# Optimization experiments

Measured on AMD Instinct MI355X. Metric: run time of the kernel, lower is better.

Reference implementation:

```python
import jax, jax.numpy as jnp
import numpy as np

B, S, H = 2, 2048, 2048
NH, KVH, HD = 32, 8, 64
G = NH // KVH
BASE = 10000.0
SCALE = 1.0 / np.sqrt(HD).astype(np.float32)


def _rope_cache(seq_len, dim, base):
    inv_freq = 1.0 / (base ** (jnp.arange(0, dim, 2, dtype=jnp.float32) / dim))
    t = jnp.arange(seq_len, dtype=jnp.float32)
    freqs = jnp.outer(t, inv_freq)            # [S, HD/2]
    emb = jnp.concatenate([freqs, freqs], -1)  # [S, HD]
    return jnp.cos(emb), jnp.sin(emb)


def _rotate_half(x):
    x1, x2 = jnp.split(x, 2, axis=-1)
    return jnp.concatenate([-x2, x1], axis=-1)


def setup_inputs() -> dict:
    key = jax.random.key(0)
    ks = jax.random.split(key, 5)
    hidden_states = jax.random.normal(ks[0], (B, S, H), jnp.float32)
    # additive causal mask, broadcast over heads
    causal = jnp.tril(jnp.ones((S, S), dtype=bool))
    attention_mask = jnp.where(causal, 0.0, -1e9).astype(jnp.float32)[None, None]
    attention_mask = jnp.broadcast_to(attention_mask, (B, 1, S, S))
    position_ids = jnp.broadcast_to(jnp.arange(S, dtype=jnp.int32), (B, S))
    w = 0.02
    Wq = jax.random.normal(ks[1], (H, NH * HD), jnp.float32) * w
    Wk = jax.random.normal(ks[2], (H, KVH * HD), jnp.float32) * w
    Wv = jax.random.normal(ks[3], (H, KVH * HD), jnp.float32) * w
    Wo = jax.random.normal(ks[4], (NH * HD, H), jnp.float32) * w
    return {"hidden_states": hidden_states, "attention_mask": attention_mask,
            "position_ids": position_ids, "Wq": Wq, "Wk": Wk, "Wv": Wv, "Wo": Wo}


def reference(hidden_states, attention_mask, position_ids, Wq, Wk, Wv, Wo):
    b, s, _ = hidden_states.shape
    q = (hidden_states @ Wq).reshape(b, s, NH, HD).transpose(0, 2, 1, 3)   # [B,NH,S,HD]
    k = (hidden_states @ Wk).reshape(b, s, KVH, HD).transpose(0, 2, 1, 3)  # [B,KVH,S,HD]
    v = (hidden_states @ Wv).reshape(b, s, KVH, HD).transpose(0, 2, 1, 3)
    cos_c, sin_c = _rope_cache(s, HD, BASE)
    cos = cos_c[position_ids][:, None]  # [B,1,S,HD]
    sin = sin_c[position_ids][:, None]
    q = q * cos + _rotate_half(q) * sin
    k = k * cos + _rotate_half(k) * sin
    # GQA: grouped einsum == repeat_kv + matmul (same math, no KV duplication)
    qg = q.reshape(b, KVH, G, s, HD)
    scores = jnp.einsum('bkgsd,bktd->bkgst', qg, k) * SCALE  # [B,KVH,G,S,S]
    scores = scores + attention_mask[:, :, None]             # mask [B,1,1,S,S]
    probs = jax.nn.softmax(scores.astype(jnp.float32), axis=-1).astype(q.dtype)
    ctx = jnp.einsum('bkgst,bktd->bkgsd', probs, v)
    ctx = ctx.reshape(b, NH, s, HD).transpose(0, 2, 1, 3).reshape(b, s, NH * HD)
    return ctx @ Wo
```

## Files before the change

kernel.cpp:

```cpp
#include <hip/hip_runtime.h>
#include <hip/hip_bf16.h>

#define DB   2
#define DS   2048
#define DH   2048
#define DNH  32
#define DKVH 8
#define DHD  64
#define DM   4096
#define DNQKV 3072

typedef __attribute__((ext_vector_type(8))) short bf16x8;
typedef __attribute__((ext_vector_type(4))) float f32x4;
typedef __attribute__((ext_vector_type(8))) unsigned short us8;
typedef __attribute__((ext_vector_type(4))) unsigned short us4;

__device__ __forceinline__ float b2f(unsigned short u) {
  unsigned int x = ((unsigned int)u) << 16;
  return __builtin_bit_cast(float, x);
}
__device__ __forceinline__ unsigned short f2b(float f) {
  unsigned int u = __builtin_bit_cast(unsigned int, f);
  return (unsigned short)((u + 0x8000u) >> 16);
}
__device__ __forceinline__ void async_copy16(void* lds, const void* g) {
  __builtin_amdgcn_global_load_lds((const __attribute__((address_space(1))) void*)g,
                                   (__attribute__((address_space(3))) void*)lds,
                                   16, 0, 0);
}

__global__ void detect_mode(const unsigned short* __restrict__ w, int* __restrict__ flags) {
  int t = threadIdx.x;
  int trips = 0;
  for (int i = 0; i < 4; i++) {
    unsigned short u = w[t * 4 + i];
    int e = (u >> 7) & 0xFF;
    if (e >= 161 || (e <= 93 && e != 0)) trips++;
  }
  for (int off = 32; off > 0; off >>= 1) trips += __shfl_down(trips, off);
  if (t == 0) flags[0] = (trips >= 8) ? 1 : 0;
}

__global__ __launch_bounds__(256) void convert_x(const void* __restrict__ xin,
                                                 unsigned short* __restrict__ xb,
                                                 const int* __restrict__ flags, int n) {
  int mode = flags[0];
  int i = (blockIdx.x * 256 + threadIdx.x) * 8;
  if (i >= n) return;
  if (mode) {
    const float* f = (const float*)xin;
    us8 o;
#pragma unroll
    for (int j = 0; j < 8; j++) o[j] = f2b(f[i + j]);
    *(us8*)&xb[i] = o;
  } else {
    *(us8*)&xb[i] = *(const us8*)((const unsigned short*)xin + i);
  }
}

__global__ __launch_bounds__(256) void transpose_w(const void* __restrict__ win,
                                                   unsigned short* __restrict__ out,
                                                   const int* __restrict__ flags,
                                                   int R, int C) {
  __shared__ float tile[32][33];
  int mode = flags[0];
  int c0 = blockIdx.x * 32, r0 = blockIdx.y * 32;
  int tx = threadIdx.x & 31, ty = threadIdx.x >> 5;
  if (mode) {
    const float* f = (const float*)win;
    for (int i = ty; i < 32; i += 8) tile[i][tx] = f[(size_t)(r0 + i) * C + c0 + tx];
  } else {
    const unsigned short* bsrc = (const unsigned short*)win;
    for (int i = ty; i < 32; i += 8) tile[i][tx] = b2f(bsrc[(size_t)(r0 + i) * C + c0 + tx]);
  }
  __syncthreads();
  for (int i = ty; i < 32; i += 8) out[(size_t)(c0 + i) * R + r0 + tx] = f2b(tile[tx][i]);
}

#define QSC 0.18033688011112042f

__global__ __launch_bounds__(256)
void gemm_qkv(const unsigned short* __restrict__ A, const unsigned short* __restrict__ Bt,
              const int* __restrict__ pos_ids,
              unsigned short* __restrict__ qws, unsigned short* __restrict__ kws,
              unsigned short* __restrict__ vt) {
  __shared__ __align__(16) unsigned short lA[2 * 128 * 32];
  __shared__ __align__(16) unsigned short lB[2 * 128 * 32];
  int tid = threadIdx.x, lane = tid & 63, wave = tid >> 6;
  int wm = wave >> 1, wn = wave & 1;
  int quad = lane >> 4, l15 = lane & 15;
  size_t tm0 = (size_t)blockIdx.y * 128, tn0 = (size_t)blockIdx.x * 128;

  f32x4 zero4 = {0.f, 0.f, 0.f, 0.f};
  f32x4 acc[4][4];
#pragma unroll
  for (int mi = 0; mi < 4; mi++)
#pragma unroll
    for (int ni = 0; ni < 4; ni++) acc[mi][ni] = zero4;

  for (int kt = 0; kt < 32; kt++) {
    __syncthreads();
#pragma unroll
    for (int i = 0; i < 4; i++) {
      int c = tid + 256 * i;
      int col = (c & 3) * 8;
      int r = (c >> 2) & 127;
      int half = c >> 9;
      async_copy16(&lA[c * 8], A + (tm0 + r) * DH + kt * 64 + half * 32 + col);
      async_copy16(&lB[c * 8], Bt + (tn0 + r) * DH + kt * 64 + half * 32 + col);
    }
    __syncthreads();
#pragma unroll
    for (int ks = 0; ks < 2; ks++) {
      bf16x8 af[4], bfr[4];
#pragma unroll
      for (int mi = 0; mi < 4; mi++)
        af[mi] = *(const bf16x8*)&lA[ks * 4096 + (wm * 64 + mi * 16 + l15) * 32 + quad * 8];
#pragma unroll
      for (int ni = 0; ni < 4; ni++)
        bfr[ni] = *(const bf16x8*)&lB[ks * 4096 + (wn * 64 + ni * 16 + l15) * 32 + quad * 8];
#pragma unroll
      for (int mi = 0; mi < 4; mi++)
#pragma unroll
        for (int ni = 0; ni < 4; ni++)
          acc[mi][ni] = __builtin_amdgcn_mfma_f32_16x16x32_bf16(af[mi], bfr[ni], acc[mi][ni], 0, 0, 0);
    }
  }

  int hs = (int)(tn0 >> 6) + wn;
  if (hs < 40) {
    float sc = (hs < 32) ? QSC : 1.0f;
    unsigned short* dst0 = (hs < 32) ? qws : kws;
    int hh = (hs < 32) ? hs : (hs - 32);
    float invf0 = __expf(-(float)l15 * (9.210340371976184f / 32.0f));
    float invf1 = invf0 * 0.01f;
#pragma unroll
    for (int mi = 0; mi < 4; mi++)
#pragma unroll
      for (int r = 0; r < 4; r++) {
        size_t gr = tm0 + wm * 64 + mi * 16 + quad * 4 + r;
        int b = (int)(gr >> 11), s = (int)(gr & 2047);
        float t = (float)pos_ids[gr];
        unsigned short* row = dst0 + ((size_t)(b * ((hs < 32) ? DNH : DKVH) + hh) * DS + s) * DHD;
#pragma unroll
        for (int ni = 0; ni < 2; ni++) {
          float x1 = acc[mi][ni][r], x2 = acc[mi][ni + 2][r];
          float ang = t * (ni ? invf1 : invf0);
          float sn, cs;
          __sincosf(ang, &sn, &cs);
          int d = ni * 16 + l15;
          row[d]      = f2b((x1 * cs - x2 * sn) * sc);
          row[d + 32] = f2b((x2 * cs + x1 * sn) * sc);
        }
      }
  } else {
    int vh = hs - 40;
    int b = (int)(tm0 >> 11);
    int s0 = (int)(tm0 & 2047) + wm * 64 + quad * 4;
#pragma unroll
    for (int mi = 0; mi < 4; mi++)
#pragma unroll
      for (int ni = 0; ni < 4; ni++) {
        int d = ni * 16 + l15;
        us4 o4;
#pragma unroll
        for (int r = 0; r < 4; r++) o4[r] = f2b(acc[mi][ni][r]);
        *(us4*)&vt[((size_t)(b * DKVH + vh) * DHD + d) * DS + s0 + mi * 16] = o4;
      }
  }
}

__global__ __launch_bounds__(256)
void gemm_out(const unsigned short* __restrict__ A, const unsigned short* __restrict__ Bt,
              unsigned short* __restrict__ Cb, float* __restrict__ Cf,
              const int* __restrict__ outmode) {
  __shared__ __align__(16) unsigned short lA[2 * 128 * 32];
  __shared__ __align__(16) unsigned short lB[2 * 128 * 32];
  int tid = threadIdx.x, lane = tid & 63, wave = tid >> 6;
  int wm = wave >> 1, wn = wave & 1;
  int quad = lane >> 4, l15 = lane & 15;
  size_t tm0 = (size_t)blockIdx.y * 128, tn0 = (size_t)blockIdx.x * 128;

  f32x4 zero4 = {0.f, 0.f, 0.f, 0.f};
  f32x4 acc[4][4];
#pragma unroll
  for (int mi = 0; mi < 4; mi++)
#pragma unroll
    for (int ni = 0; ni < 4; ni++) acc[mi][ni] = zero4;

  for (int kt = 0; kt < 32; kt++) {
    __syncthreads();
#pragma unroll
    for (int i = 0; i < 4; i++) {
      int c = tid + 256 * i;
      int col = (c & 3) * 8;
      int r = (c >> 2) & 127;
      int half = c >> 9;
      async_copy16(&lA[c * 8], A + (tm0 + r) * DH + kt * 64 + half * 32 + col);
      async_copy16(&lB[c * 8], Bt + (tn0 + r) * DH + kt * 64 + half * 32 + col);
    }
    __syncthreads();
#pragma unroll
    for (int ks = 0; ks < 2; ks++) {
      bf16x8 af[4], bfr[4];
#pragma unroll
      for (int mi = 0; mi < 4; mi++)
        af[mi] = *(const bf16x8*)&lA[ks * 4096 + (wm * 64 + mi * 16 + l15) * 32 + quad * 8];
#pragma unroll
      for (int ni = 0; ni < 4; ni++)
        bfr[ni] = *(const bf16x8*)&lB[ks * 4096 + (wn * 64 + ni * 16 + l15) * 32 + quad * 8];
#pragma unroll
      for (int mi = 0; mi < 4; mi++)
#pragma unroll
        for (int ni = 0; ni < 4; ni++)
          acc[mi][ni] = __builtin_amdgcn_mfma_f32_16x16x32_bf16(af[mi], bfr[ni], acc[mi][ni], 0, 0, 0);
    }
  }
  int mode = *outmode;
#pragma unroll
  for (int mi = 0; mi < 4; mi++)
#pragma unroll
    for (int ni = 0; ni < 4; ni++)
#pragma unroll
      for (int r = 0; r < 4; r++) {
        size_t gr = tm0 + wm * 64 + mi * 16 + quad * 4 + r;
        size_t gc = tn0 + wn * 64 + ni * 16 + l15;
        float v = acc[mi][ni][r];
        if (mode) Cf[gr * DH + gc] = v;
        else      Cb[gr * DH + gc] = f2b(v);
      }
}

__global__ __launch_bounds__(256, 4)
void flash_attn(const unsigned short* __restrict__ q, const unsigned short* __restrict__ k,
                const unsigned short* __restrict__ vt, unsigned short* __restrict__ ctx) {
  __shared__ __align__(16) unsigned short lK0[64 * 32];
  __shared__ __align__(16) unsigned short lK1[64 * 32];
  __shared__ __align__(16) unsigned short lV0[64 * 32];
  __shared__ __align__(16) unsigned short lV1[64 * 32];
  __shared__ __align__(16) unsigned short lP[4 * 16 * 72];
  int tid = threadIdx.x, lane = tid & 63, wave = tid >> 6;
  int quad = lane >> 4, l15 = lane & 15;
  int bh = blockIdx.y, b = bh >> 5, h = bh & 31, kvh = h >> 2;
  const unsigned short* qb = q + (size_t)(b * DNH + h) * DS * DHD;
  const unsigned short* kb = k + (size_t)(b * DKVH + kvh) * DS * DHD;
  const unsigned short* vb = vt + (size_t)(b * DKVH + kvh) * DHD * DS;
  unsigned short* lPw = lP + wave * 16 * 72;
  int r4 = tid >> 2, c8 = (tid & 3) * 8;

  f32x4 zero4 = {0.f, 0.f, 0.f, 0.f};
  for (int ph = 0; ph < 2; ph++) {
    int qt = ph ? (31 - blockIdx.x) : blockIdx.x;
    int q0 = qt * 64;
    const unsigned short* qp = qb + (size_t)(q0 + wave * 16 + l15) * DHD + quad * 8;
    bf16x8 qf0 = *(const bf16x8*)qp;
    bf16x8 qf1 = *(const bf16x8*)(qp + 32);
    f32x4 oacc[4];
#pragma unroll
    for (int dj = 0; dj < 4; dj++) oacc[dj] = zero4;
    float mrow = -1e30f, lrow = 0.f;

    int nt = qt + 1;
    for (int t = 0; t < nt; t++) {
      int kv0 = t * 64;
      __syncthreads();
      async_copy16(&lK0[tid * 8], kb + (size_t)(kv0 + r4) * DHD + c8);
      async_copy16(&lK1[tid * 8], kb + (size_t)(kv0 + r4) * DHD + 32 + c8);
      async_copy16(&lV0[tid * 8], vb + (size_t)r4 * DS + kv0 + c8);
      async_copy16(&lV1[tid * 8], vb + (size_t)r4 * DS + kv0 + 32 + c8);
      __syncthreads();

      f32x4 sacc[4];
#pragma unroll
      for (int nj = 0; nj < 4; nj++) {
        sacc[nj] = zero4;
        bf16x8 kf0 = *(const bf16x8*)&lK0[(nj * 16 + l15) * 32 + quad * 8];
        bf16x8 kf1 = *(const bf16x8*)&lK1[(nj * 16 + l15) * 32 + quad * 8];
        sacc[nj] = __builtin_amdgcn_mfma_f32_16x16x32_bf16(kf0, qf0, sacc[nj], 0, 0, 0);
        sacc[nj] = __builtin_amdgcn_mfma_f32_16x16x32_bf16(kf1, qf1, sacc[nj], 0, 0, 0);
      }
      if (t == nt - 1) {
        int ql = wave * 16 + l15;
#pragma unroll
        for (int nj = 0; nj < 4; nj++)
#pragma unroll
          for (int r = 0; r < 4; r++)
            if (nj * 16 + quad * 4 + r > ql) sacc[nj][r] = -1e30f;
      }
      float tm = -1e30f;
#pragma unroll
      for (int nj = 0; nj < 4; nj++)
#pragma unroll
        for (int r = 0; r < 4; r++) tm = fmaxf(tm, sacc[nj][r]);
      tm = fmaxf(tm, __shfl_xor(tm, 16));
      tm = fmaxf(tm, __shfl_xor(tm, 32));
      float mn = fmaxf(mrow, tm);
      float alpha = __builtin_amdgcn_exp2f(mrow - mn);
      mrow = mn;
      float rs = 0.f;
      float p[4][4];
#pragma unroll
      for (int nj = 0; nj < 4; nj++)
#pragma unroll
        for (int r = 0; r < 4; r++) {
          float e = __builtin_amdgcn_exp2f(sacc[nj][r] - mn);
          p[nj][r] = e;
          rs += e;
        }
      rs += __shfl_xor(rs, 16);
      rs += __shfl_xor(rs, 32);
      lrow = lrow * alpha + rs;
#pragma unroll
      for (int nj = 0; nj < 4; nj++) {
        us4 w4;
#pragma unroll
        for (int r = 0; r < 4; r++) w4[r] = f2b(p[nj][r]);
        *(us4*)&lPw[l15 * 72 + nj * 16 + quad * 4] = w4;
      }
      bf16x8 pf0 = *(const bf16x8*)&lPw[l15 * 72 + quad * 8];
      bf16x8 pf1 = *(const bf16x8*)&lPw[l15 * 72 + 32 + quad * 8];
#pragma unroll
      for (int dj = 0; dj < 4; dj++) {
#pragma unroll
        for (int r = 0; r < 4; r++) oacc[dj][r] *= alpha;
        bf16x8 vf0 = *(const bf16x8*)&lV0[(dj * 16 + l15) * 32 + quad * 8];
        bf16x8 vf1 = *(const bf16x8*)&lV1[(dj * 16 + l15) * 32 + quad * 8];
        oacc[dj] = __builtin_amdgcn_mfma_f32_16x16x32_bf16(vf0, pf0, oacc[dj], 0, 0, 0);
        oacc[dj] = __builtin_amdgcn_mfma_f32_16x16x32_bf16(vf1, pf1, oacc[dj], 0, 0, 0);
      }
    }
    float inv = __builtin_amdgcn_rcpf(lrow);
    size_t orow = ((size_t)b * DS + q0 + wave * 16 + l15) * (DNH * DHD) + (size_t)h * DHD;
#pragma unroll
    for (int dj = 0; dj < 4; dj++) {
      us4 o4;
#pragma unroll
      for (int r = 0; r < 4; r++) o4[r] = f2b(oacc[dj][r] * inv);
      *(us4*)&ctx[orow + dj * 16 + quad * 4] = o4;
    }
  }
}

extern "C" void kernel_launch(void* const* d_in, const int* in_sizes, int n_in,
                              void* d_out, int out_size, void* d_ws, size_t ws_size,
                              hipStream_t stream) {
  (void)in_sizes; (void)n_in; (void)out_size; (void)ws_size;
  const void* hs = d_in[0];
  const int* pos = (const int*)d_in[2];
  const void* wq = d_in[3];
  const void* wk = d_in[4];
  const void* wv = d_in[5];
  const void* wo = d_in[6];

  char* ws = (char*)d_ws;
  size_t off = 0;
  auto take = [&](size_t bytes) -> char* {
    char* p = ws + off;
    off += (bytes + 255) & ~(size_t)255;
    return p;
  };
  int* flags            = (int*)take(256);
  unsigned short* xb    = (unsigned short*)take((size_t)DM * DH * 2);
  unsigned short* wtqkv = (unsigned short*)take((size_t)DNQKV * DH * 2);
  unsigned short* wto   = (unsigned short*)take((size_t)DH * DH * 2);
  unsigned short* qws   = (unsigned short*)take((size_t)DB * DNH * DS * DHD * 2);
  unsigned short* kws   = (unsigned short*)take((size_t)DB * DKVH * DS * DHD * 2);
  unsigned short* vtws  = (unsigned short*)take((size_t)DB * DKVH * DS * DHD * 2);
  unsigned short* ctx   = (unsigned short*)take((size_t)DM * DNH * DHD * 2);

  detect_mode<<<1, 64, 0, stream>>>((const unsigned short*)wq, flags);
  convert_x<<<DM * DH / 8 / 256, 256, 0, stream>>>(hs, xb, flags, DM * DH);
  transpose_w<<<dim3(64, 64), 256, 0, stream>>>(wq, wtqkv, flags, 2048, 2048);
  transpose_w<<<dim3(16, 64), 256, 0, stream>>>(wk, wtqkv + (size_t)2048 * 2048, flags, 2048, 512);
  transpose_w<<<dim3(16, 64), 256, 0, stream>>>(wv, wtqkv + (size_t)2560 * 2048, flags, 2048, 512);
  transpose_w<<<dim3(64, 64), 256, 0, stream>>>(wo, wto, flags, 2048, 2048);

  gemm_qkv<<<dim3(24, 32), 256, 0, stream>>>(xb, wtqkv, pos, qws, kws, vtws);

  flash_attn<<<dim3(16, DB * DNH), 256, 0, stream>>>(qws, kws, vtws, ctx);

  gemm_out<<<dim3(16, 32), 256, 0, stream>>>(ctx, wto, (unsigned short*)d_out, (float*)d_out, flags);
}
```

Measured before the change: 357.1 us.

## Rewrite QKV and output GEMMs with larger tiles and pipelined double-buffered LDS

Both projection GEMMs move to 512-thread blocks with larger tiles (256x256 for QKV, 128x256 for output). Global-to-LDS loads are double-buffered across K-steps and split into half-tiles interleaved with MFMA phases, using explicit vmcnt waits and s_setprio. The change also adds an XOR swizzle on LDS to avoid bank conflicts and remaps block IDs for L2 locality. It aims to hide memory latency and raise MFMA utilization. The cost is many barriers, heavy register pressure (acc[8][4] in QKV) and fewer blocks (192 and 256), which may leave CUs idle.

```diff
diff --git a/kernel.cpp b/kernel.cpp
--- a/kernel.cpp
+++ b/kernel.cpp
@@ -28,6 +28,11 @@
                                    (__attribute__((address_space(3))) void*)lds,
                                    16, 0, 0);
 }
+
+#define BARRIER() do { asm volatile("" ::: "memory"); __builtin_amdgcn_s_barrier(); asm volatile("" ::: "memory"); } while (0)
+#define LGKM0()   asm volatile("s_waitcnt lgkmcnt(0)" ::: "memory")
+#define WAITVM(n) asm volatile("s_waitcnt vmcnt(" #n ")" ::: "memory")
+#define MFMA16(d, a, bb) (d) = __builtin_amdgcn_mfma_f32_16x16x32_bf16((a), (bb), (d), 0, 0, 0)
 
 __global__ void detect_mode(const unsigned short* __restrict__ w, int* __restrict__ flags) {
   int t = threadIdx.x;
@@ -79,53 +84,115 @@
 
 #define QSC 0.18033688011112042f
 
-__global__ __launch_bounds__(256)
+__global__ __launch_bounds__(512, 2)
 void gemm_qkv(const unsigned short* __restrict__ A, const unsigned short* __restrict__ Bt,
               const int* __restrict__ pos_ids,
               unsigned short* __restrict__ qws, unsigned short* __restrict__ kws,
               unsigned short* __restrict__ vt) {
-  __shared__ __align__(16) unsigned short lA[2 * 128 * 32];
-  __shared__ __align__(16) unsigned short lB[2 * 128 * 32];
+  __shared__ __align__(16) unsigned short sm[65536];
   int tid = threadIdx.x, lane = tid & 63, wave = tid >> 6;
-  int wm = wave >> 1, wn = wave & 1;
+  int wm = wave >> 2, wn = wave & 3;
   int quad = lane >> 4, l15 = lane & 15;
-  size_t tm0 = (size_t)blockIdx.y * 128, tn0 = (size_t)blockIdx.x * 128;
+
+  int bid = blockIdx.x;
+  int wg = (bid & 7) * 24 + (bid >> 3);
+  int ty = wg / 12, tx = wg - ty * 12;
+  size_t tm0 = (size_t)ty * 256, tn0 = (size_t)tx * 256;
+
+  const unsigned short* Ab = A + tm0 * 2048;
+  const unsigned short* Bb = Bt + tn0 * 2048;
+
+  auto UA = [&](int bu, int kh) { return sm + (bu * 2 + kh) * 8192; };
+  auto UB = [&](int bu, int kh) { return sm + 32768 + (bu * 2 + kh) * 8192; };
+
+  int c0 = tid, c1 = tid + 512;
+  int r0s = c0 >> 2, r1s = c1 >> 2;
+  int cc0 = (c0 & 3) ^ ((r0s >> 1) & 3);
+  int cc1 = (c1 & 3) ^ ((r1s >> 1) & 3);
+  size_t ga0 = (size_t)r0s * 2048 + cc0 * 8;
+  size_t ga1 = (size_t)r1s * 2048 + cc1 * 8;
+
+  auto stA = [&](int t, int kh, int bu) {
+    const unsigned short* s = Ab + (size_t)t * 64 + kh * 32;
+    async_copy16(UA(bu, kh) + c0 * 8, s + ga0);
+    async_copy16(UA(bu, kh) + c1 * 8, s + ga1);
+  };
+  auto stB = [&](int t, int kh, int bu) {
+    const unsigned short* s = Bb + (size_t)t * 64 + kh * 32;
+    async_copy16(UB(bu, kh) + c0 * 8, s + ga0);
+    async_copy16(UB(bu, kh) + c1 * 8, s + ga1);
+  };
+
+  int rdoff = l15 * 32 + ((quad << 3) ^ (((l15 >> 1) & 3) << 3));
 
   f32x4 zero4 = {0.f, 0.f, 0.f, 0.f};
-  f32x4 acc[4][4];
-#pragma unroll
-  for (int mi = 0; mi < 4; mi++)
+  f32x4 acc[8][4];
+#pragma unroll
+  for (int mi = 0; mi < 8; mi++)
 #pragma unroll
     for (int ni = 0; ni < 4; ni++) acc[mi][ni] = zero4;
 
-  for (int kt = 0; kt < 32; kt++) {
-    __syncthreads();
-#pragma unroll
-    for (int i = 0; i < 4; i++) {
-      int c = tid + 256 * i;
-      int col = (c & 3) * 8;
-      int r = (c >> 2) & 127;
-      int half = c >> 9;
-      async_copy16(&lA[c * 8], A + (tm0 + r) * DH + kt * 64 + half * 32 + col);
-      async_copy16(&lB[c * 8], Bt + (tn0 + r) * DH + kt * 64 + half * 32 + col);
-    }
-    __syncthreads();
-#pragma unroll
-    for (int ks = 0; ks < 2; ks++) {
-      bf16x8 af[4], bfr[4];
-#pragma unroll
-      for (int mi = 0; mi < 4; mi++)
-        af[mi] = *(const bf16x8*)&lA[ks * 4096 + (wm * 64 + mi * 16 + l15) * 32 + quad * 8];
-#pragma unroll
-      for (int ni = 0; ni < 4; ni++)
-        bfr[ni] = *(const bf16x8*)&lB[ks * 4096 + (wn * 64 + ni * 16 + l15) * 32 + quad * 8];
-#pragma unroll
-      for (int mi = 0; mi < 4; mi++)
-#pragma unroll
-        for (int ni = 0; ni < 4; ni++)
-          acc[mi][ni] = __builtin_amdgcn_mfma_f32_16x16x32_bf16(af[mi], bfr[ni], acc[mi][ni], 0, 0, 0);
-    }
-  }
+  stA(0, 0, 0); stB(0, 0, 0); stA(0, 1, 0); stB(0, 1, 0); stA(1, 0, 1); stB(1, 0, 1);
+  WAITVM(8); BARRIER();
+
+#pragma unroll 2
+  for (int t = 0; t < 32; ++t) {
+    int bu = t & 1, bn = bu ^ 1;
+    int t1 = (t + 1 < 32) ? t + 1 : 31;
+    int t2 = (t + 2 < 32) ? t + 2 : 31;
+    bf16x8 af[8];
+    const unsigned short* pA0 = UA(bu, 0) + wm * 4096 + rdoff;
+    const unsigned short* pB0 = UB(bu, 0) + wn * 2048 + rdoff;
+    const unsigned short* pA1 = UA(bu, 1) + wm * 4096 + rdoff;
+    const unsigned short* pB1 = UB(bu, 1) + wn * 2048 + rdoff;
+
+#pragma unroll
+    for (int mi = 0; mi < 8; mi++) af[mi] = *(const bf16x8*)(pA0 + mi * 512);
+    bf16x8 b0 = *(const bf16x8*)pB0;
+    bf16x8 b1 = *(const bf16x8*)(pB0 + 512);
+    stA(t1, 1, bn);
+    BARRIER(); LGKM0();
+    __builtin_amdgcn_s_setprio(1);
+#pragma unroll
+    for (int mi = 0; mi < 8; mi++) { MFMA16(acc[mi][0], af[mi], b0); MFMA16(acc[mi][1], af[mi], b1); }
+    __builtin_amdgcn_s_setprio(0);
+    BARRIER();
+
+    bf16x8 b2 = *(const bf16x8*)(pB0 + 1024);
+    bf16x8 b3 = *(const bf16x8*)(pB0 + 1536);
+    stB(t1, 1, bn);
+    BARRIER(); LGKM0();
+    __builtin_amdgcn_s_setprio(1);
+#pragma unroll
+    for (int mi = 0; mi < 8; mi++) { MFMA16(acc[mi][2], af[mi], b2); MFMA16(acc[mi][3], af[mi], b3); }
+    __builtin_amdgcn_s_setprio(0);
+    WAITVM(8);
+    BARRIER();
+
+#pragma unroll
+    for (int mi = 0; mi < 8; mi++) af[mi] = *(const bf16x8*)(pA1 + mi * 512);
+    b0 = *(const bf16x8*)pB1;
+    b1 = *(const bf16x8*)(pB1 + 512);
+    stA(t2, 0, bu);
+    BARRIER(); LGKM0();
+    __builtin_amdgcn_s_setprio(1);
+#pragma unroll
+    for (int mi = 0; mi < 8; mi++) { MFMA16(acc[mi][0], af[mi], b0); MFMA16(acc[mi][1], af[mi], b1); }
+    __builtin_amdgcn_s_setprio(0);
+    BARRIER();
+
+    b2 = *(const bf16x8*)(pB1 + 1024);
+    b3 = *(const bf16x8*)(pB1 + 1536);
+    stB(t2, 0, bu);
+    BARRIER(); LGKM0();
+    __builtin_amdgcn_s_setprio(1);
+#pragma unroll
+    for (int mi = 0; mi < 8; mi++) { MFMA16(acc[mi][2], af[mi], b2); MFMA16(acc[mi][3], af[mi], b3); }
+    __builtin_amdgcn_s_setprio(0);
+    WAITVM(8);
+    BARRIER();
+  }
+  WAITVM(0);
 
   int hs = (int)(tn0 >> 6) + wn;
   if (hs < 40) {
@@ -135,17 +202,17 @@
     float invf0 = __expf(-(float)l15 * (9.210340371976184f / 32.0f));
     float invf1 = invf0 * 0.01f;
 #pragma unroll
-    for (int mi = 0; mi < 4; mi++)
+    for (int mi = 0; mi < 8; mi++)
 #pragma unroll
       for (int r = 0; r < 4; r++) {
-        size_t gr = tm0 + wm * 64 + mi * 16 + quad * 4 + r;
-        int b = (int)(gr >> 11), s = (int)(gr & 2047);
-        float t = (float)pos_ids[gr];
-        unsigned short* row = dst0 + ((size_t)(b * ((hs < 32) ? DNH : DKVH) + hh) * DS + s) * DHD;
+        size_t gr = tm0 + wm * 128 + mi * 16 + quad * 4 + r;
+        int bb = (int)(gr >> 11), s = (int)(gr & 2047);
+        float tpos = (float)pos_ids[gr];
+        unsigned short* row = dst0 + ((size_t)(bb * ((hs < 32) ? DNH : DKVH) + hh) * DS + s) * DHD;
 #pragma unroll
         for (int ni = 0; ni < 2; ni++) {
           float x1 = acc[mi][ni][r], x2 = acc[mi][ni + 2][r];
-          float ang = t * (ni ? invf1 : invf0);
+          float ang = tpos * (ni ? invf1 : invf0);
           float sn, cs;
           __sincosf(ang, &sn, &cs);
           int d = ni * 16 + l15;
@@ -155,31 +222,59 @@
       }
   } else {
     int vh = hs - 40;
-    int b = (int)(tm0 >> 11);
-    int s0 = (int)(tm0 & 2047) + wm * 64 + quad * 4;
-#pragma unroll
-    for (int mi = 0; mi < 4; mi++)
+    int bb = (int)(tm0 >> 11);
+    int s0 = (int)(tm0 & 2047) + wm * 128 + quad * 4;
+#pragma unroll
+    for (int mi = 0; mi < 8; mi++)
 #pragma unroll
       for (int ni = 0; ni < 4; ni++) {
         int d = ni * 16 + l15;
         us4 o4;
 #pragma unroll
         for (int r = 0; r < 4; r++) o4[r] = f2b(acc[mi][ni][r]);
-        *(us4*)&vt[((size_t)(b * DKVH + vh) * DHD + d) * DS + s0 + mi * 16] = o4;
-      }
-  }
-}
-
-__global__ __launch_bounds__(256)
+        *(us4*)&vt[((size_t)(bb * DKVH + vh) * DHD + d) * DS + s0 + mi * 16] = o4;
+      }
+  }
+}
+
+__global__ __launch_bounds__(512, 2)
 void gemm_out(const unsigned short* __restrict__ A, const unsigned short* __restrict__ Bt,
               unsigned short* __restrict__ Cb, float* __restrict__ Cf,
               const int* __restrict__ outmode) {
-  __shared__ __align__(16) unsigned short lA[2 * 128 * 32];
-  __shared__ __align__(16) unsigned short lB[2 * 128 * 32];
+  __shared__ __align__(16) unsigned short sm[49152];
   int tid = threadIdx.x, lane = tid & 63, wave = tid >> 6;
-  int wm = wave >> 1, wn = wave & 1;
+  int wm = wave >> 2, wn = wave & 3;
   int quad = lane >> 4, l15 = lane & 15;
-  size_t tm0 = (size_t)blockIdx.y * 128, tn0 = (size_t)blockIdx.x * 128;
+
+  int bid = blockIdx.x;
+  int wg = (bid & 7) * 32 + (bid >> 3);
+  int ty = wg >> 3, tx = wg & 7;
+  size_t tm0 = (size_t)ty * 128, tn0 = (size_t)tx * 256;
+
+  const unsigned short* Ab = A + tm0 * 2048;
+  const unsigned short* Bb = Bt + tn0 * 2048;
+
+  auto UA = [&](int bu, int kh) { return sm + (bu * 2 + kh) * 4096; };
+  auto UB = [&](int bu, int kh) { return sm + 16384 + (bu * 2 + kh) * 8192; };
+
+  int c0 = tid, c1 = tid + 512;
+  int r0s = c0 >> 2, r1s = c1 >> 2;
+  int cc0 = (c0 & 3) ^ ((r0s >> 1) & 3);
+  int cc1 = (c1 & 3) ^ ((r1s >> 1) & 3);
+  size_t ga0 = (size_t)r0s * 2048 + cc0 * 8;
+  size_t ga1 = (size_t)r1s * 2048 + cc1 * 8;
+
+  auto stA = [&](int t, int kh, int bu) {
+    const unsigned short* s = Ab + (size_t)t * 64 + kh * 32;
+    async_copy16(UA(bu, kh) + c0 * 8, s + ga0);
+  };
+  auto stB = [&](int t, int kh, int bu) {
+    const unsigned short* s = Bb + (size_t)t * 64 + kh * 32;
+    async_copy16(UB(bu, kh) + c0 * 8, s + ga0);
+    async_copy16(UB(bu, kh) + c1 * 8, s + ga1);
+  };
+
+  int rdoff = l15 * 32 + ((quad << 3) ^ (((l15 >> 1) & 3) << 3));
 
   f32x4 zero4 = {0.f, 0.f, 0.f, 0.f};
   f32x4 acc[4][4];
@@ -188,34 +283,68 @@
 #pragma unroll
     for (int ni = 0; ni < 4; ni++) acc[mi][ni] = zero4;
 
-  for (int kt = 0; kt < 32; kt++) {
-    __syncthreads();
-#pragma unroll
-    for (int i = 0; i < 4; i++) {
-      int c = tid + 256 * i;
-      int col = (c & 3) * 8;
-      int r = (c >> 2) & 127;
-      int half = c >> 9;
-      async_copy16(&lA[c * 8], A + (tm0 + r) * DH + kt * 64 + half * 32 + col);
-      async_copy16(&lB[c * 8], Bt + (tn0 + r) * DH + kt * 64 + half * 32 + col);
-    }
-    __syncthreads();
-#pragma unroll
-    for (int ks = 0; ks < 2; ks++) {
-      bf16x8 af[4], bfr[4];
-#pragma unroll
-      for (int mi = 0; mi < 4; mi++)
-        af[mi] = *(const bf16x8*)&lA[ks * 4096 + (wm * 64 + mi * 16 + l15) * 32 + quad * 8];
-#pragma unroll
-      for (int ni = 0; ni < 4; ni++)
-        bfr[ni] = *(const bf16x8*)&lB[ks * 4096 + (wn * 64 + ni * 16 + l15) * 32 + quad * 8];
-#pragma unroll
-      for (int mi = 0; mi < 4; mi++)
-#pragma unroll
-        for (int ni = 0; ni < 4; ni++)
-          acc[mi][ni] = __builtin_amdgcn_mfma_f32_16x16x32_bf16(af[mi], bfr[ni], acc[mi][ni], 0, 0, 0);
-    }
-  }
+  stA(0, 0, 0); stB(0, 0, 0); stA(0, 1, 0); stB(0, 1, 0); stA(1, 0, 1); stB(1, 0, 1);
+  WAITVM(6); BARRIER();
+
+#pragma unroll 2
+  for (int t = 0; t < 32; ++t) {
+    int bu = t & 1, bn = bu ^ 1;
+    int t1 = (t + 1 < 32) ? t + 1 : 31;
+    int t2 = (t + 2 < 32) ? t + 2 : 31;
+    bf16x8 af[4];
+    const unsigned short* pA0 = UA(bu, 0) + wm * 2048 + rdoff;
+    const unsigned short* pB0 = UB(bu, 0) + wn * 2048 + rdoff;
+    const unsigned short* pA1 = UA(bu, 1) + wm * 2048 + rdoff;
+    const unsigned short* pB1 = UB(bu, 1) + wn * 2048 + rdoff;
+
+#pragma unroll
+    for (int mi = 0; mi < 4; mi++) af[mi] = *(const bf16x8*)(pA0 + mi * 512);
+    bf16x8 b0 = *(const bf16x8*)pB0;
+    bf16x8 b1 = *(const bf16x8*)(pB0 + 512);
+    stA(t1, 1, bn);
+    BARRIER(); LGKM0();
+    __builtin_amdgcn_s_setprio(1);
+#pragma unroll
+    for (int mi = 0; mi < 4; mi++) { MFMA16(acc[mi][0], af[mi], b0); MFMA16(acc[mi][1], af[mi], b1); }
+    __builtin_amdgcn_s_setprio(0);
+    BARRIER();
+
+    bf16x8 b2 = *(const bf16x8*)(pB0 + 1024);
+    bf16x8 b3 = *(const bf16x8*)(pB0 + 1536);
+    stB(t1, 1, bn);
+    BARRIER(); LGKM0();
+    __builtin_amdgcn_s_setprio(1);
+#pragma unroll
+    for (int mi = 0; mi < 4; mi++) { MFMA16(acc[mi][2], af[mi], b2); MFMA16(acc[mi][3], af[mi], b3); }
+    __builtin_amdgcn_s_setprio(0);
+    WAITVM(6);
+    BARRIER();
+
+#pragma unroll
+    for (int mi = 0; mi < 4; mi++) af[mi] = *(const bf16x8*)(pA1 + mi * 512);
+    b0 = *(const bf16x8*)pB1;
+    b1 = *(const bf16x8*)(pB1 + 512);
+    stA(t2, 0, bu);
+    BARRIER(); LGKM0();
+    __builtin_amdgcn_s_setprio(1);
+#pragma unroll
+    for (int mi = 0; mi < 4; mi++) { MFMA16(acc[mi][0], af[mi], b0); MFMA16(acc[mi][1], af[mi], b1); }
+    __builtin_amdgcn_s_setprio(0);
+    BARRIER();
+
+    b2 = *(const bf16x8*)(pB1 + 1024);
+    b3 = *(const bf16x8*)(pB1 + 1536);
+    stB(t2, 0, bu);
+    BARRIER(); LGKM0();
+    __builtin_amdgcn_s_setprio(1);
+#pragma unroll
+    for (int mi = 0; mi < 4; mi++) { MFMA16(acc[mi][2], af[mi], b2); MFMA16(acc[mi][3], af[mi], b3); }
+    __builtin_amdgcn_s_setprio(0);
+    WAITVM(6);
+    BARRIER();
+  }
+  WAITVM(0);
+
   int mode = *outmode;
 #pragma unroll
   for (int mi = 0; mi < 4; mi++)
@@ -226,8 +355,8 @@
         size_t gr = tm0 + wm * 64 + mi * 16 + quad * 4 + r;
         size_t gc = tn0 + wn * 64 + ni * 16 + l15;
         float v = acc[mi][ni][r];
-        if (mode) Cf[gr * DH + gc] = v;
-        else      Cb[gr * DH + gc] = f2b(v);
+        if (mode) Cf[gr * 2048 + gc] = v;
+        else      Cb[gr * 2048 + gc] = f2b(v);
       }
 }
 
@@ -375,9 +504,9 @@
   transpose_w<<<dim3(16, 64), 256, 0, stream>>>(wv, wtqkv + (size_t)2560 * 2048, flags, 2048, 512);
   transpose_w<<<dim3(64, 64), 256, 0, stream>>>(wo, wto, flags, 2048, 2048);
 
-  gemm_qkv<<<dim3(24, 32), 256, 0, stream>>>(xb, wtqkv, pos, qws, kws, vtws);
+  gemm_qkv<<<dim3(192), 512, 0, stream>>>(xb, wtqkv, pos, qws, kws, vtws);
 
   flash_attn<<<dim3(16, DB * DNH), 256, 0, stream>>>(qws, kws, vtws, ctx);
 
-  gemm_out<<<dim3(16, 32), 256, 0, stream>>>(ctx, wto, (unsigned short*)d_out, (float*)d_out, flags);
-}
+  gemm_out<<<dim3(256), 512, 0, stream>>>(ctx, wto, (unsigned short*)d_out, (float*)d_out, flags);
+}
```

Result: faster. 329.3 us (-7.8%).
